# Optimization experiments

Measured on AMD Instinct MI355X. Metric: run time of the kernel, lower is better.

The kernel has to match this reference:

```python
import jax, jax.numpy as jnp
import numpy as np

# ---- exact Hungarian (Jonker-Volgenant / e-maxx shortest augmenting path) ----

def _lsa(cost):
    """Square cost matrix [n,n] (numpy) -> col index assigned to each row (optimal)."""
    n = cost.shape[0]
    a = np.zeros((n + 1, n + 1), dtype=np.float64)
    a[1:, 1:] = cost
    u = np.zeros(n + 1)
    v = np.zeros(n + 1)
    p = np.zeros(n + 1, dtype=np.int64)   # p[j] = row matched to column j (1-indexed)
    way = np.zeros(n + 1, dtype=np.int64)
    for i in range(1, n + 1):
        p[0] = i
        j0 = 0
        minv = np.full(n + 1, np.inf)
        used = np.zeros(n + 1, dtype=bool)
        while True:
            used[j0] = True
            i0 = p[j0]
            cur = a[i0] - u[i0] - v
            better = (~used) & (cur < minv)
            minv[better] = cur[better]
            way[better] = j0
            masked = np.where(used, np.inf, minv)
            j1 = int(np.argmin(masked))
            delta = masked[j1]
            u[p[used]] += delta
            v[used] -= delta
            minv[~used] -= delta
            j0 = j1
            if p[j0] == 0:
                break
        while j0 != 0:
            j1 = way[j0]
            p[j0] = p[j1]
            j0 = j1
    col = np.zeros(n, dtype=np.int64)
    for j in range(1, n + 1):
        col[p[j] - 1] = j - 1
    return col


def _lsa_batch(costs):
    """costs [..., N, N] numpy -> assigned col per row [..., N]."""
    N = costs.shape[-1]
    flat = costs.reshape(-1, N, N)
    cols = np.stack([_lsa(c) for c in flat])
    return cols.reshape(costs.shape[:-1])


# ---- kernel pieces (same math as cdist_torch / material_distances) ----

def _pair_sqdist(v1, v2):
    g = jnp.einsum('pnd,bmd->pbnm', v1, v2)
    s1 = (v1 ** 2).sum(-1)
    s2 = (v2 ** 2).sum(-1)
    return jnp.abs(-2.0 * g + s1[:, None, :, None] + s2[None, :, None, :])


def _self_sqdist(v):
    # v [B,N,d] -> [B,N,N]; only diagonal pairs of Material_kernel(x,x) are needed
    g = jnp.einsum('bnd,bmd->bnm', v, v)
    s = (v ** 2).sum(-1)
    return jnp.abs(-2.0 * g + s[:, :, None] + s[:, None, :])


def _material_kernel(D2, cols):
    # sum_i exp(-D2[..., i, cols[..., i]]) / N  (Hungarian-matched similarity)
    sel = jnp.take_along_axis(D2, cols[..., None], axis=-1)[..., 0]
    return jnp.exp(-sel).sum(-1) / D2.shape[-1]


def setup_inputs():
    key = jax.random.key(0)
    ks = jax.random.split(key, 4)
    P, B, A, d = 64, 32, 40, 128
    x = jax.random.normal(ks[0], (B, A, d), jnp.float32)
    data_points = jax.random.normal(ks[1], (P, A, d), jnp.float32)
    gamma = jnp.full((1, d), -2.0, jnp.float32)  # matches __init__: ones(1,n_in)*-2
    M = jax.random.normal(ks[2], (P, P), jnp.float32)
    K = M @ M.T + P * jnp.eye(P, dtype=jnp.float32)
    L = jnp.linalg.cholesky(K).astype(jnp.float32)  # valid trained-state Cholesky buffer
    alpha = jax.random.normal(ks[3], (P,), jnp.float32)
    return {"x": x, "data_points": data_points, "gamma": gamma, "L": L, "alpha": alpha}


def reference(x, data_points, gamma, L, alpha):
    g = jnp.exp(gamma)                      # [1,d]
    v1 = data_points * g                    # [P,A,d]
    v2 = x * g                              # [B,A,d]
    D2 = _pair_sqdist(v1, v2)               # [P,B,A,A]
    cols = jnp.asarray(_lsa_batch(np.asarray(D2, np.float64)))
    K_xnew = _material_kernel(D2, cols)     # [P,B]
    Linv = jnp.linalg.inv(L)
    v = Linv @ K_xnew                       # [P,B]
    mean = jnp.einsum('in,i->n', K_xnew, alpha)
    Ds = _self_sqdist(v2)                   # [B,A,A] (diagonal of K(x,x) only)
    cols_s = jnp.asarray(_lsa_batch(np.asarray(Ds, np.float64)))
    kxx = _material_kernel(Ds, cols_s)      # [B]
    var = kxx - jnp.einsum('in,in->n', v, v)
    return mean, var
```

## Files before the change

kernel.cpp:

```cpp
#include <hip/hip_runtime.h>
#include <math.h>

#define P_N 64
#define B_N 32
#define A_N 40
#define D_N 128

__device__ __forceinline__ int readlane_i(int v, int l) {
  return __builtin_amdgcn_readlane(v, l);
}
__device__ __forceinline__ float readlane_f(float v, int l) {
  return __int_as_float(__builtin_amdgcn_readlane(__float_as_int(v), l));
}
__device__ __forceinline__ unsigned ordf(float f) {
  unsigned b = __float_as_uint(f);
  return b ^ (((unsigned)((int)b >> 31)) | 0x80000000u);
}
__device__ __forceinline__ unsigned wave_min_u32(unsigned x) {
  unsigned t;
  t = (unsigned)__builtin_amdgcn_update_dpp((int)0xFFFFFFFFu, (int)x, 0x111, 0xF, 0xF, false);
  x = t < x ? t : x;
  t = (unsigned)__builtin_amdgcn_update_dpp((int)0xFFFFFFFFu, (int)x, 0x112, 0xF, 0xF, false);
  x = t < x ? t : x;
  t = (unsigned)__builtin_amdgcn_update_dpp((int)0xFFFFFFFFu, (int)x, 0x114, 0xF, 0xF, false);
  x = t < x ? t : x;
  t = (unsigned)__builtin_amdgcn_update_dpp((int)0xFFFFFFFFu, (int)x, 0x118, 0xF, 0xF, false);
  x = t < x ? t : x;
  t = (unsigned)__builtin_amdgcn_update_dpp((int)0xFFFFFFFFu, (int)x, 0x142, 0xA, 0xF, false);
  x = t < x ? t : x;
  t = (unsigned)__builtin_amdgcn_update_dpp((int)0xFFFFFFFFu, (int)x, 0x143, 0xC, 0xF, false);
  x = t < x ? t : x;
  return (unsigned)__builtin_amdgcn_readlane((int)x, 63);
}

__global__ __launch_bounds__(64) void hungarian_pair(
    const float* __restrict__ DP, const float* __restrict__ X,
    const float* __restrict__ G, float* __restrict__ out) {
  __shared__ float Cs[A_N * A_N];
  __shared__ float g_lds[D_N];
  const int bid  = blockIdx.x;
  const int lane = threadIdx.x;
  const float* __restrict__ Abase = DP + (bid >> 5) * (A_N * D_N);
  const float* __restrict__ Bbase = X  + (bid & 31) * (A_N * D_N);

  g_lds[lane]      = expf(G[lane]);
  g_lds[lane + 64] = expf(G[lane + 64]);
  __syncthreads();

  if (lane < A_N) {
    const float* bp = Bbase + lane * D_N;
    for (int c = 0; c < 4; ++c) {
      float4 gg[8], bb[8];
      #pragma unroll
      for (int k = 0; k < 8; ++k) {
        gg[k] = ((const float4*)(g_lds + c * 32))[k];
        float4 br = ((const float4*)(bp + c * 32))[k];
        bb[k] = make_float4(br.x * gg[k].x, br.y * gg[k].y,
                            br.z * gg[k].z, br.w * gg[k].w);
      }
      for (int i = 0; i < A_N; ++i) {
        const float4* ap = (const float4*)(Abase + i * D_N + c * 32);
        float s = 0.f;
        #pragma unroll
        for (int k = 0; k < 8; ++k) {
          float4 a = ap[k];
          float dx = fmaf(a.x, gg[k].x, -bb[k].x); s = fmaf(dx, dx, s);
          float dy = fmaf(a.y, gg[k].y, -bb[k].y); s = fmaf(dy, dy, s);
          float dz = fmaf(a.z, gg[k].z, -bb[k].z); s = fmaf(dz, dz, s);
          float dw = fmaf(a.w, gg[k].w, -bb[k].w); s = fmaf(dw, dw, s);
        }
        if (c == 0) Cs[i * A_N + lane] = s;
        else        Cs[i * A_N + lane] += s;
      }
    }
  }
  __syncthreads();

  const int  cix     = (lane >= 1 && lane <= A_N) ? (lane - 1) : 0;
  const bool realcol = (lane >= 1 && lane <= A_N);

  float vpot = 0.f;
  int   amin = 0;
  if (realcol) {
    float mn = INFINITY; int mi = 0;
    for (int i = 0; i < A_N; ++i) {
      float c = Cs[i * A_N + cix];
      if (c < mn) { mn = c; mi = i; }
    }
    vpot = mn; amin = mi + 1;
  }

  unsigned long long rmask = 0ull;
  int p = 0, way = 0;
  for (int j = 1; j <= A_N; ++j) {
    int am = readlane_i(amin, j);
    if (!((rmask >> am) & 1ull)) {
      rmask |= 1ull << am;
      if (lane == j) p = am;
    }
  }

  float u = 0.f;

  for (int i = 1; i <= A_N; ++i) {
    if ((rmask >> i) & 1ull) continue;
    float r = realcol ? (Cs[(i - 1) * A_N + cix] - vpot) : INFINITY;
    unsigned key = (ordf(r) & 0xFFFFFFC0u) | (unsigned)lane;
    unsigned kmin = wave_min_u32(key);
    int jm = (int)(kmin & 63u);
    int pj = readlane_i(p, jm);
    if (pj == 0) {
      float rmin = readlane_f(r, jm);
      if (lane == jm) p = i;
      if (lane == i)  u = rmin;
      rmask |= 1ull << i;
    }
  }

  for (int f = 1; f <= A_N; ++f) {
    if ((rmask >> f) & 1ull) continue;
    if (lane == 0) p = f;
    float mhat = INFINITY;
    float excl = realcol ? 0.f : INFINITY;
    float dsum = 0.f;
    float dent = 0.f, rent = 0.f;
    bool  used   = !realcol;
    bool  intree = (lane == f);
    int   j0 = 0, i0 = f;
    const unsigned plane_key = ((unsigned)p << 6) | (unsigned)lane;
    for (int guard = 0; guard < 42; ++guard) {
      float Craw = Cs[(i0 - 1) * A_N + cix];
      float uc   = readlane_f(u, i0);
      float off  = dsum - uc - vpot + excl;
      float cand = Craw + off;
      if (cand < mhat) way = j0;
      mhat = fminf(mhat, cand);
      unsigned key = (ordf(mhat) & 0xFFFFF000u) | plane_key;
      unsigned kmin = wave_min_u32(key);
      int j1 = (int)(kmin & 63u);
      int i1 = (int)((kmin >> 6) & 63u);
      float dnew = readlane_f(mhat, j1);
      if (lane == j1) { used = true; dent = dnew; excl = INFINITY; mhat = INFINITY; }
      dsum = dnew;
      j0 = j1;
      i0 = i1;
      if (i1 == 0) break;
      if (lane == i1) { intree = true; rent = dnew; }
    }
    if (used && realcol) vpot -= (dsum - dent);
    if (intree)          u    += (dsum - rent);
    while (j0 != 0) {
      int jn = readlane_i(way, j0);
      int pn = readlane_i(p, jn);
      if (lane == j0) p = pn;
      j0 = jn;
    }
  }

  float e = 0.f;
  if (realcol) e = expf(-Cs[(p - 1) * A_N + (lane - 1)]);
  #pragma unroll
  for (int off = 32; off; off >>= 1) e += __shfl_xor(e, off);
  if (lane == 0) out[bid] = e / 40.0f;
}

__global__ __launch_bounds__(64) void final_kernel(
    const float* __restrict__ Kx, const float* __restrict__ L,
    const float* __restrict__ alpha, float* __restrict__ out) {
  __shared__ float vl[P_N * B_N];
  int b = threadIdx.x;
  if (b >= B_N) return;
  float mean = 0.f;
  for (int p = 0; p < P_N; ++p) mean = fmaf(Kx[p * B_N + b], alpha[p], mean);
  out[b] = mean;
  float sumv2 = 0.f;
  for (int i = 0; i < P_N; ++i) {
    float s = Kx[i * B_N + b];
    for (int j = 0; j < i; ++j) s = fmaf(-L[i * P_N + j], vl[j * B_N + b], s);
    float vi = s / L[i * P_N + i];
    vl[i * B_N + b] = vi;
    sumv2 = fmaf(vi, vi, sumv2);
  }
  out[B_N + b] = 1.0f - sumv2;
}

extern "C" void kernel_launch(void* const* d_in, const int* in_sizes, int n_in,
                              void* d_out, int out_size, void* d_ws, size_t ws_size,
                              hipStream_t stream) {
  const float* x     = (const float*)d_in[0];
  const float* dp    = (const float*)d_in[1];
  const float* gamma = (const float*)d_in[2];
  const float* L     = (const float*)d_in[3];
  const float* alpha = (const float*)d_in[4];
  float* out = (float*)d_out;

  float* Kx = (float*)d_ws;

  hungarian_pair<<<P_N * B_N, 64, 0, stream>>>(dp, x, gamma, Kx);
  final_kernel<<<1, 64, 0, stream>>>(Kx, L, alpha, out);
}
```

Baseline: 153.7 us.

## Keep per-column cost matrix in registers instead of LDS for Hungarian solve

Each lane now holds its whole cost column (40 floats) in registers and no longer stores it in a shared-memory matrix. Lookups use a wave-uniform switch-based select (sel40_u) or a per-lane mux tree (sel40_v). This removes LDS writes, the barrier and LDS reads on the serial augmenting-path loop, trading them for select instructions and much higher register pressure. The launch-bounds occupancy hint is also set to 2.

```diff
diff --git a/kernel.cpp b/kernel.cpp
--- a/kernel.cpp
+++ b/kernel.cpp
@@ -33,13 +33,47 @@
   return (unsigned)__builtin_amdgcn_readlane((int)x, 63);
 }
 
-__global__ __launch_bounds__(64) void hungarian_pair(
+__device__ __forceinline__ float mux8(float r0, float r1, float r2, float r3,
+                                      float r4, float r5, float r6, float r7, int k) {
+  float a = (k & 1) ? r1 : r0;
+  float b = (k & 1) ? r3 : r2;
+  float c = (k & 1) ? r5 : r4;
+  float d = (k & 1) ? r7 : r6;
+  float e = (k & 2) ? b : a;
+  float f = (k & 2) ? d : c;
+  return (k & 4) ? f : e;
+}
+__device__ __forceinline__ float sel40_u(const float (&R)[A_N], int k) {
+  int kk = k & 7;
+  switch (k >> 3) {
+    case 0:  return mux8(R[0],  R[1],  R[2],  R[3],  R[4],  R[5],  R[6],  R[7],  kk);
+    case 1:  return mux8(R[8],  R[9],  R[10], R[11], R[12], R[13], R[14], R[15], kk);
+    case 2:  return mux8(R[16], R[17], R[18], R[19], R[20], R[21], R[22], R[23], kk);
+    case 3:  return mux8(R[24], R[25], R[26], R[27], R[28], R[29], R[30], R[31], kk);
+    default: return mux8(R[32], R[33], R[34], R[35], R[36], R[37], R[38], R[39], kk);
+  }
+}
+__device__ __forceinline__ float sel40_v(const float (&R)[A_N], int k) {
+  int kk = k & 7, g = k >> 3;
+  float m0 = mux8(R[0],  R[1],  R[2],  R[3],  R[4],  R[5],  R[6],  R[7],  kk);
+  float m1 = mux8(R[8],  R[9],  R[10], R[11], R[12], R[13], R[14], R[15], kk);
+  float m2 = mux8(R[16], R[17], R[18], R[19], R[20], R[21], R[22], R[23], kk);
+  float m3 = mux8(R[24], R[25], R[26], R[27], R[28], R[29], R[30], R[31], kk);
+  float m4 = mux8(R[32], R[33], R[34], R[35], R[36], R[37], R[38], R[39], kk);
+  float t01 = (g & 1) ? m1 : m0;
+  float t23 = (g & 1) ? m3 : m2;
+  float t   = (g & 2) ? t23 : t01;
+  return (g & 4) ? m4 : t;
+}
+
+__global__ __launch_bounds__(64, 2) void hungarian_pair(
     const float* __restrict__ DP, const float* __restrict__ X,
     const float* __restrict__ G, float* __restrict__ out) {
-  __shared__ float Cs[A_N * A_N];
   __shared__ float g_lds[D_N];
   const int bid  = blockIdx.x;
   const int lane = threadIdx.x;
+  const bool realcol = (lane >= 1 && lane <= A_N);
+  const int  cix     = realcol ? (lane - 1) : 0;
   const float* __restrict__ Abase = DP + (bid >> 5) * (A_N * D_N);
   const float* __restrict__ Bbase = X  + (bid & 31) * (A_N * D_N);
 
@@ -47,8 +81,11 @@
   g_lds[lane + 64] = expf(G[lane + 64]);
   __syncthreads();
 
-  if (lane < A_N) {
-    const float* bp = Bbase + lane * D_N;
+  float Creg[A_N];
+  #pragma unroll
+  for (int i = 0; i < A_N; ++i) Creg[i] = 0.f;
+  if (realcol) {
+    const float* bp = Bbase + cix * D_N;
     for (int c = 0; c < 4; ++c) {
       float4 gg[8], bb[8];
       #pragma unroll
@@ -58,6 +95,7 @@
         bb[k] = make_float4(br.x * gg[k].x, br.y * gg[k].y,
                             br.z * gg[k].z, br.w * gg[k].w);
       }
+      #pragma unroll
       for (int i = 0; i < A_N; ++i) {
         const float4* ap = (const float4*)(Abase + i * D_N + c * 32);
         float s = 0.f;
@@ -69,23 +107,18 @@
           float dz = fmaf(a.z, gg[k].z, -bb[k].z); s = fmaf(dz, dz, s);
           float dw = fmaf(a.w, gg[k].w, -bb[k].w); s = fmaf(dw, dw, s);
         }
-        if (c == 0) Cs[i * A_N + lane] = s;
-        else        Cs[i * A_N + lane] += s;
+        Creg[i] += s;
       }
     }
   }
-  __syncthreads();
-
-  const int  cix     = (lane >= 1 && lane <= A_N) ? (lane - 1) : 0;
-  const bool realcol = (lane >= 1 && lane <= A_N);
 
   float vpot = 0.f;
   int   amin = 0;
   if (realcol) {
-    float mn = INFINITY; int mi = 0;
-    for (int i = 0; i < A_N; ++i) {
-      float c = Cs[i * A_N + cix];
-      if (c < mn) { mn = c; mi = i; }
+    float mn = Creg[0]; int mi = 0;
+    #pragma unroll
+    for (int i = 1; i < A_N; ++i) {
+      if (Creg[i] < mn) { mn = Creg[i]; mi = i; }
     }
     vpot = mn; amin = mi + 1;
   }
@@ -104,7 +137,7 @@
 
   for (int i = 1; i <= A_N; ++i) {
     if ((rmask >> i) & 1ull) continue;
-    float r = realcol ? (Cs[(i - 1) * A_N + cix] - vpot) : INFINITY;
+    float r = realcol ? (sel40_u(Creg, i - 1) - vpot) : INFINITY;
     unsigned key = (ordf(r) & 0xFFFFFFC0u) | (unsigned)lane;
     unsigned kmin = wave_min_u32(key);
     int jm = (int)(kmin & 63u);
@@ -129,7 +162,7 @@
     int   j0 = 0, i0 = f;
     const unsigned plane_key = ((unsigned)p << 6) | (unsigned)lane;
     for (int guard = 0; guard < 42; ++guard) {
-      float Craw = Cs[(i0 - 1) * A_N + cix];
+      float Craw = sel40_u(Creg, i0 - 1);
       float uc   = readlane_f(u, i0);
       float off  = dsum - uc - vpot + excl;
       float cand = Craw + off;
@@ -157,8 +190,9 @@
     }
   }
 
-  float e = 0.f;
-  if (realcol) e = expf(-Cs[(p - 1) * A_N + (lane - 1)]);
+  int   pk = realcol ? (p - 1) : 0;
+  float cm = sel40_v(Creg, pk);
+  float e  = realcol ? expf(-cm) : 0.f;
   #pragma unroll
   for (int off = 32; off; off >>= 1) e += __shfl_xor(e, off);
   if (lane == 0) out[bid] = e / 40.0f;
```

After: 192.4 us. 25.2% more time.
